# Kernel tuning notes

Measured on AMD Instinct MI355X. Metric: run time of the kernel, lower is better.

Reference implementation:

```python
import jax, jax.numpy as jnp
import numpy as np


def setup_inputs() -> dict:
    key = jax.random.key(0)
    k1, k2, k3 = jax.random.split(key, 3)
    B, T, D, Uh = 64, 256, 1024, 1024
    x = jax.random.normal(k1, (B, T, D), dtype=jnp.float32)
    W = jax.random.normal(k2, (D, 4 * Uh), dtype=jnp.float32) * 0.02
    U = jax.random.normal(k3, (Uh, 4 * Uh), dtype=jnp.float32) * 0.02
    b = jnp.zeros((4 * Uh,), dtype=jnp.float32)
    return {"x": x, "W": W, "U": U, "b": b}


def _lstm(x, W, U, b):
    # Keras LSTM, inference mode (dropout inactive). Gate order: i, f, c, o.
    B = x.shape[0]
    units = U.shape[0]
    # Precompute input projection for all timesteps: [B,T,4U] -> scan over T.
    xz = jnp.einsum('btd,dg->btg', x, W) + b
    xz = jnp.swapaxes(xz, 0, 1)  # [T,B,4U]

    def step(carry, xz_t):
        h, c = carry
        z = xz_t + h @ U  # [B,4U]
        zi, zf, zg, zo = jnp.split(z, 4, axis=-1)
        i = jax.nn.sigmoid(zi)
        f = jax.nn.sigmoid(zf)
        g = jnp.tanh(zg)
        o = jax.nn.sigmoid(zo)
        c_new = f * c + i * g
        h_new = o * jnp.tanh(c_new)
        return (h_new, c_new), h_new

    h0 = jnp.zeros((B, units), dtype=x.dtype)
    c0 = jnp.zeros((B, units), dtype=x.dtype)
    _, hs = jax.lax.scan(step, (h0, c0), xz)  # hs: [T,B,U]
    return jnp.swapaxes(hs, 0, 1)  # [B,T,U] (return_sequences=True)


def reference(x, W, U, b):
    return _lstm(x, W, U, b)
```

## Files before the change

### kernel.cpp

```cpp
#include <hip/hip_runtime.h>
#include <cstdint>
#include <cstddef>

typedef __attribute__((ext_vector_type(8))) short short8;
typedef __attribute__((ext_vector_type(4))) short short4v;
typedef __attribute__((ext_vector_type(4))) float f32x4;

static constexpr int B_ = 64, T_ = 256, D_ = 1024, NH = 1024, NG = 4096;
static constexpr int NBLK = 64;
static constexpr int LDS_BYTES = 131072 + 16384 + 64;

__device__ __forceinline__ short f2bs(float f) {
  union { float f; uint32_t u; } cv; cv.f = f;
  uint32_t u = cv.u;
  uint32_t r = (u + 0x7fffu + ((u >> 16) & 1u)) >> 16;
  return (short)(uint16_t)r;
}
__device__ __forceinline__ float bs2f(short s) {
  union { uint32_t u; float f; } cv; cv.u = ((uint32_t)(uint16_t)s) << 16; return cv.f;
}
__device__ __forceinline__ float fsigm(float x) {
  return __builtin_amdgcn_rcpf(1.f + __expf(-x));
}
__device__ __forceinline__ float ftanh(float x) {
  return 1.f - 2.f * __builtin_amdgcn_rcpf(__expf(2.f * x) + 1.f);
}

__global__ __launch_bounds__(256) void xz_gemm(const float* __restrict__ x,
                                               const float* __restrict__ W,
                                               const float* __restrict__ bias,
                                               short* __restrict__ xzT)
{
  constexpr int BM = 128, BN = 128, BK = 32;
  __shared__ short As[BM][BK];
  __shared__ short Bs[BK][BN];
  __shared__ short Cs[BM][136];
  const int tid  = threadIdx.x;
  const int lane = tid & 63, wave = tid >> 6;
  const int wm = (wave >> 1) * 64, wn = (wave & 1) * 64;
  const int fr = lane & 15, kg = lane >> 4;
  const int bm = blockIdx.x * BM, bn = blockIdx.y * BN;

  f32x4 acc[4][4] = {};

  for (int k0 = 0; k0 < D_; k0 += BK) {
    {
      const int r0 = tid >> 3, kq = (tid & 7) * 4;
      #pragma unroll
      for (int it = 0; it < 4; ++it) {
        const int row = r0 + it * 32;
        const float4 v = *reinterpret_cast<const float4*>(&x[(size_t)(bm + row) * D_ + k0 + kq]);
        short4v s; s.x = f2bs(v.x); s.y = f2bs(v.y); s.z = f2bs(v.z); s.w = f2bs(v.w);
        *reinterpret_cast<short4v*>(&As[row][kq]) = s;
      }
    }
    {
      const int kr0 = tid >> 5, nq = (tid & 31) * 4;
      #pragma unroll
      for (int it = 0; it < 4; ++it) {
        const int krow = kr0 + it * 8;
        const float4 v = *reinterpret_cast<const float4*>(&W[(size_t)(k0 + krow) * NG + bn + nq]);
        short4v s; s.x = f2bs(v.x); s.y = f2bs(v.y); s.z = f2bs(v.z); s.w = f2bs(v.w);
        *reinterpret_cast<short4v*>(&Bs[krow][nq]) = s;
      }
    }
    __syncthreads();

    short8 af[4];
    #pragma unroll
    for (int mi = 0; mi < 4; ++mi)
      af[mi] = *reinterpret_cast<const short8*>(&As[wm + mi * 16 + fr][kg * 8]);
    #pragma unroll
    for (int ni = 0; ni < 4; ++ni) {
      short8 bf;
      #pragma unroll
      for (int j = 0; j < 8; ++j) bf[j] = Bs[kg * 8 + j][wn + ni * 16 + fr];
      #pragma unroll
      for (int mi = 0; mi < 4; ++mi)
        acc[mi][ni] = __builtin_amdgcn_mfma_f32_16x16x32_bf16(af[mi], bf, acc[mi][ni], 0, 0, 0);
    }
    __syncthreads();
  }

  const int fq = lane >> 4;
  #pragma unroll
  for (int ni = 0; ni < 4; ++ni) {
    const int coln = wn + ni * 16 + fr;
    const float bv = bias[bn + coln];
    #pragma unroll
    for (int mi = 0; mi < 4; ++mi) {
      const int rowb = wm + mi * 16 + fq * 4;
      #pragma unroll
      for (int r = 0; r < 4; ++r)
        Cs[rowb + r][coln] = f2bs(acc[mi][ni][r] + bv);
    }
  }
  __syncthreads();

  const int bb  = bm >> 8;
  const int t0  = bm & 255;
  const int g   = bn >> 10;
  const int rb0 = (bn & 1023) >> 4;
  #pragma unroll
  for (int it = 0; it < 4; ++it) {
    const int cid  = it * 256 + tid;
    const int trow = cid >> 3, uu = cid & 7;
    short* dst = xzT + ((size_t)((rb0 + uu) * 256 + (t0 + trow)) * 64 + bb) * 64 + g * 16;
    const short8 v0 = *reinterpret_cast<const short8*>(&Cs[trow][uu * 16]);
    const short8 v1 = *reinterpret_cast<const short8*>(&Cs[trow][uu * 16 + 8]);
    *reinterpret_cast<short8*>(dst)     = v0;
    *reinterpret_cast<short8*>(dst + 8) = v1;
  }
}

#define H_ISSUE(BUF, O0,O1,O2,O3,O4,O5,O6,O7) \
  asm volatile( \
    "global_load_dwordx4 %0, %8, off offset:" #O0 " sc0 sc1\n\t" \
    "global_load_dwordx4 %1, %8, off offset:" #O1 " sc0 sc1\n\t" \
    "global_load_dwordx4 %2, %8, off offset:" #O2 " sc0 sc1\n\t" \
    "global_load_dwordx4 %3, %8, off offset:" #O3 " sc0 sc1\n\t" \
    "global_load_dwordx4 %4, %8, off offset:" #O4 " sc0 sc1\n\t" \
    "global_load_dwordx4 %5, %8, off offset:" #O5 " sc0 sc1\n\t" \
    "global_load_dwordx4 %6, %8, off offset:" #O6 " sc0 sc1" \
    "\n\tglobal_load_dwordx4 %7, %8, off offset:" #O7 " sc0 sc1" \
    : "=&v"(BUF[0]), "=&v"(BUF[1]), "=&v"(BUF[2]), "=&v"(BUF[3]), \
      "=&v"(BUF[4]), "=&v"(BUF[5]), "=&v"(BUF[6]), "=&v"(BUF[7]) \
    : "v"(hp) : "memory")

#define WAITV(N) do { asm volatile("s_waitcnt vmcnt(" #N ")" ::: "memory"); \
                      __builtin_amdgcn_sched_barrier(0); } while (0)

#define LDSWAIT(C) do { \
    while (__hip_atomic_load(&go[C], __ATOMIC_RELAXED, __HIP_MEMORY_SCOPE_WORKGROUP) < t) \
      __builtin_amdgcn_s_sleep(1); \
    __builtin_amdgcn_sched_barrier(0); \
  } while (0)

#define MFMA_CHUNK(BUF, CH) \
  { _Pragma("unroll") \
    for (int i = 0; i < 8; ++i) { \
      const int ksAbs = kh * 16 + (CH) * 8 + i; \
      _Pragma("unroll") \
      for (int nt = 0; nt < 4; ++nt) { \
        const int so = ((ksAbs * 4 + kg) * 64 + nt * 16 + fr) * 8; \
        const short8 bf = *reinterpret_cast<const short8*>(&Us[so]); \
        acc[nt] = __builtin_amdgcn_mfma_f32_16x16x32_bf16(BUF[i], bf, acc[nt], 0, 0, 0); \
      } \
    } }

__global__ __launch_bounds__(576) void lstm_persist(const short* __restrict__ xzT,
                                                    const float* __restrict__ U,
                                                    short* __restrict__ h0buf,
                                                    short* __restrict__ h1buf,
                                                    int* __restrict__ flags,
                                                    float* __restrict__ out)
{
  extern __shared__ char smem[];
  short* Us  = (short*)smem;
  float* zsm = (float*)(smem + 131072);
  int*   go  = (int*)(smem + 131072 + 16384);

  const int tid  = threadIdx.x;
  const int lane = tid & 63, wave = tid >> 6;
  const int bid  = blockIdx.x;
  const int u0   = bid * 16;
  const int fr = lane & 15, kg = lane >> 4;
  const int mt = wave & 3;
  const int kh = wave >> 2;
  const int gb = tid >> 3, gup = tid & 7;

  for (int idx = tid; idx < 1024 * 64; idx += 576) {
    const int k = idx >> 6, c = idx & 63;
    const float v = U[(size_t)k * NG + (c >> 4) * NH + u0 + (c & 15)];
    Us[((k >> 3) * 64 + c) * 8 + (k & 7)] = f2bs(v);
  }
  if (tid < 4) go[tid] = 0;
  float creg0 = 0.f, creg1 = 0.f;
  __syncthreads();

  for (int t = 0; t < T_; ++t) {
    const short* __restrict__ hprev = (t & 1) ? h0buf : h1buf;
    short* __restrict__ hnext       = (t & 1) ? h1buf : h0buf;

    int xzw[4];
    if (tid < 512) {
      const short* xb = xzT + (((size_t)bid * 256 + t) * 64 + gb) * 64;
      #pragma unroll
      for (int g = 0; g < 4; ++g)
        xzw[g] = *reinterpret_cast<const int*>(xb + g * 16 + 2 * gup);
    }

    f32x4 acc[4] = {};
    if (t > 0) {
      if (wave == 8) {
        const int* fp = flags + lane * 16;
        uint32_t pub = 0;
        while (pub != 0xFu) {
          const int v = __hip_atomic_load(fp, __ATOMIC_RELAXED, __HIP_MEMORY_SCOPE_AGENT);
          const unsigned long long rdy = __ballot(v >= t);
          #pragma unroll
          for (int c = 0; c < 4; ++c) {
            if (!((pub >> c) & 1u) && (((rdy >> (c * 16)) & 0xFFFFull) == 0xFFFFull)) {
              if (lane == (unsigned)(c * 16))
                __hip_atomic_store(&go[c], t, __ATOMIC_RELAXED, __HIP_MEMORY_SCOPE_WORKGROUP);
              pub |= 1u << c;
            }
          }
          if (pub != 0xFu) __builtin_amdgcn_s_sleep(1);
        }
      } else {
        const short* hp = hprev + (size_t)(mt * 16 + fr) * NH + kh * 512 + kg * 8;
        short8 ha[8], hb[8];
        LDSWAIT(2 * kh);     H_ISSUE(ha, 0, 64, 128, 192, 256, 320, 384, 448);
        LDSWAIT(2 * kh + 1); H_ISSUE(hb, 512, 576, 640, 704, 768, 832, 896, 960);
        WAITV(8);  MFMA_CHUNK(ha, 0);
        WAITV(0);  MFMA_CHUNK(hb, 1);
        if (kh == 1) {
          #pragma unroll
          for (int nt = 0; nt < 4; ++nt)
            #pragma unroll
            for (int r = 0; r < 4; ++r)
              zsm[(mt * 16 + kg * 4 + r) * 64 + nt * 16 + fr] = acc[nt][r];
        }
      }
      __syncthreads();
      if (wave < 8 && kh == 0) {
        #pragma unroll
        for (int nt = 0; nt < 4; ++nt)
          #pragma unroll
          for (int r = 0; r < 4; ++r) {
            const int zi = (mt * 16 + kg * 4 + r) * 64 + nt * 16 + fr;
            zsm[zi] += acc[nt][r];
          }
      }
      __syncthreads();
    }

    float hh0 = 0.f, hh1 = 0.f;
    if (tid < 512) {
      float z[4][2];
      #pragma unroll
      for (int g = 0; g < 4; ++g) {
        z[g][0] = bs2f((short)(xzw[g] & 0xFFFF));
        z[g][1] = bs2f((short)(((uint32_t)xzw[g]) >> 16));
        if (t > 0) {
          const float2 zz = *reinterpret_cast<const float2*>(&zsm[gb * 64 + g * 16 + 2 * gup]);
          z[g][0] += zz.x; z[g][1] += zz.y;
        }
      }
      {
        const float ig = fsigm(z[0][0]), fg = fsigm(z[1][0]);
        const float gg = ftanh(z[2][0]), og = fsigm(z[3][0]);
        creg0 = fg * creg0 + ig * gg;  hh0 = og * ftanh(creg0);
      }
      {
        const float ig = fsigm(z[0][1]), fg = fsigm(z[1][1]);
        const float gg = ftanh(z[2][1]), og = fsigm(z[3][1]);
        creg1 = fg * creg1 + ig * gg;  hh1 = og * ftanh(creg1);
      }
      if (t < T_ - 1) {
        const uint32_t word = (uint32_t)(uint16_t)f2bs(hh0) | ((uint32_t)(uint16_t)f2bs(hh1) << 16);
        uint32_t* hp32 = (uint32_t*)(hnext + (size_t)gb * NH + u0 + 2 * gup);
        asm volatile("global_store_dword %0, %1, off sc0 sc1" :: "v"(hp32), "v"(word) : "memory");
      }
    }
    if (t < T_ - 1) WAITV(0);
    __syncthreads();

    if (t < T_ - 1 && tid == 0)
      __hip_atomic_store(&flags[bid * 16], t + 1, __ATOMIC_RELAXED, __HIP_MEMORY_SCOPE_AGENT);

    if (tid < 512) {
      float2 o; o.x = hh0; o.y = hh1;
      *reinterpret_cast<float2*>(&out[((size_t)gb * T_ + t) * NH + u0 + 2 * gup]) = o;
    }
  }
}

extern "C" void kernel_launch(void* const* d_in, const int* in_sizes, int n_in,
                              void* d_out, int out_size, void* d_ws, size_t ws_size,
                              hipStream_t stream) {
  const float* x    = (const float*)d_in[0];
  const float* W    = (const float*)d_in[1];
  const float* U    = (const float*)d_in[2];
  const float* bias = (const float*)d_in[3];
  float* out = (float*)d_out;
  char* ws = (char*)d_ws;

  short* xzT   = (short*)ws;
  int*   flags = (int*)(ws + 134217728);
  short* hA    = (short*)(ws + 134225920);
  short* hB    = (short*)(ws + 134356992);

  hipMemsetAsync(flags, 0, 8192, stream);
  xz_gemm<<<dim3(128, 32), 256, 0, stream>>>(x, W, bias, xzT);

  hipFuncSetAttribute((const void*)lstm_persist,
                      hipFuncAttributeMaxDynamicSharedMemorySize, LDS_BYTES);
  lstm_persist<<<dim3(NBLK), dim3(576), LDS_BYTES, stream>>>(xzT, U, hA, hB, flags, out);
}
```

Baseline: 2.109 ms.

## Replace flag-based inter-block sync with timestep-tagged h values polled directly

Removes the per-block flag array and the dedicated polling wave. Each stored h value now carries the timestep in its upper 16 bits, and consumers spin-reload their h fragments until every tag matches. This drops the store-drain wait, the extra block barrier and the flag round-trip on the recurrent critical path, at the cost of doubling the h buffer size and repacking loaded words into bf16 operands. It also pads the z scratch rows to 68 floats to reduce LDS bank conflicts and shrinks the block to 512 threads.

After: 2.292 ms. +8.7%, slower.

```diff
diff --git a/kernel.cpp b/kernel.cpp
--- a/kernel.cpp
+++ b/kernel.cpp
@@ -5,10 +5,12 @@
 typedef __attribute__((ext_vector_type(8))) short short8;
 typedef __attribute__((ext_vector_type(4))) short short4v;
 typedef __attribute__((ext_vector_type(4))) float f32x4;
+typedef __attribute__((ext_vector_type(4))) int int4v;
+typedef __attribute__((ext_vector_type(2))) int int2v;
 
 static constexpr int B_ = 64, T_ = 256, D_ = 1024, NH = 1024, NG = 4096;
 static constexpr int NBLK = 64;
-static constexpr int LDS_BYTES = 131072 + 16384 + 64;
+static constexpr int LDS_BYTES = 131072 + 64 * 68 * 4;
 
 __device__ __forceinline__ short f2bs(float f) {
   union { float f; uint32_t u; } cv; cv.f = f;
@@ -113,52 +115,50 @@
   }
 }
 
-#define H_ISSUE(BUF, O0,O1,O2,O3,O4,O5,O6,O7) \
-  asm volatile( \
-    "global_load_dwordx4 %0, %8, off offset:" #O0 " sc0 sc1\n\t" \
-    "global_load_dwordx4 %1, %8, off offset:" #O1 " sc0 sc1\n\t" \
-    "global_load_dwordx4 %2, %8, off offset:" #O2 " sc0 sc1\n\t" \
-    "global_load_dwordx4 %3, %8, off offset:" #O3 " sc0 sc1\n\t" \
-    "global_load_dwordx4 %4, %8, off offset:" #O4 " sc0 sc1\n\t" \
-    "global_load_dwordx4 %5, %8, off offset:" #O5 " sc0 sc1\n\t" \
-    "global_load_dwordx4 %6, %8, off offset:" #O6 " sc0 sc1" \
-    "\n\tglobal_load_dwordx4 %7, %8, off offset:" #O7 " sc0 sc1" \
-    : "=&v"(BUF[0]), "=&v"(BUF[1]), "=&v"(BUF[2]), "=&v"(BUF[3]), \
-      "=&v"(BUF[4]), "=&v"(BUF[5]), "=&v"(BUF[6]), "=&v"(BUF[7]) \
-    : "v"(hp) : "memory")
-
 #define WAITV(N) do { asm volatile("s_waitcnt vmcnt(" #N ")" ::: "memory"); \
                       __builtin_amdgcn_sched_barrier(0); } while (0)
 
-#define LDSWAIT(C) do { \
-    while (__hip_atomic_load(&go[C], __ATOMIC_RELAXED, __HIP_MEMORY_SCOPE_WORKGROUP) < t) \
-      __builtin_amdgcn_s_sleep(1); \
-    __builtin_amdgcn_sched_barrier(0); \
-  } while (0)
-
-#define MFMA_CHUNK(BUF, CH) \
-  { _Pragma("unroll") \
-    for (int i = 0; i < 8; ++i) { \
-      const int ksAbs = kh * 16 + (CH) * 8 + i; \
-      _Pragma("unroll") \
-      for (int nt = 0; nt < 4; ++nt) { \
-        const int so = ((ksAbs * 4 + kg) * 64 + nt * 16 + fr) * 8; \
-        const short8 bf = *reinterpret_cast<const short8*>(&Us[so]); \
-        acc[nt] = __builtin_amdgcn_mfma_f32_16x16x32_bf16(BUF[i], bf, acc[nt], 0, 0, 0); \
-      } \
-    } }
-
-__global__ __launch_bounds__(576) void lstm_persist(const short* __restrict__ xzT,
-                                                    const float* __restrict__ U,
-                                                    short* __restrict__ h0buf,
-                                                    short* __restrict__ h1buf,
-                                                    int* __restrict__ flags,
-                                                    float* __restrict__ out)
+#define HL2(B0, B1, VO) \
+  asm volatile("global_load_dwordx4 %0, %2, %3 sc0 sc1\n\t" \
+               "global_load_dwordx4 %1, %2, %3 offset:16 sc0 sc1" \
+               : "=&v"(B0), "=&v"(B1) : "v"(VO), "s"(hpv) : "memory")
+
+#define ISSUE_A { _Pragma("unroll") \
+  for (int K = 0; K < 8; ++K) HL2(bufA[2*K], bufA[2*K+1], voff0 + K * 8192); }
+#define ISSUE_B { _Pragma("unroll") \
+  for (int K = 0; K < 8; ++K) HL2(bufB[2*K], bufB[2*K+1], voff0 + 65536 + K * 8192); }
+
+#define CHECKBUF(BUF) { _Pragma("unroll") \
+  for (int i = 0; i < 16; ++i) { \
+    bad |= ((uint32_t)BUF[i][0] ^ tgw); bad |= ((uint32_t)BUF[i][1] ^ tgw); \
+    bad |= ((uint32_t)BUF[i][2] ^ tgw); bad |= ((uint32_t)BUF[i][3] ^ tgw); \
+  } bad &= 0xFFFF0000u; }
+
+#define MFMA_SUB(BUF, KB) { _Pragma("unroll") \
+  for (int K = 0; K < 8; ++K) { \
+    int4v pk; \
+    pk[0] = (BUF[2*K][0]   & 0xFFFF) | (BUF[2*K][1]   << 16); \
+    pk[1] = (BUF[2*K][2]   & 0xFFFF) | (BUF[2*K][3]   << 16); \
+    pk[2] = (BUF[2*K+1][0] & 0xFFFF) | (BUF[2*K+1][1] << 16); \
+    pk[3] = (BUF[2*K+1][2] & 0xFFFF) | (BUF[2*K+1][3] << 16); \
+    const short8 fa = __builtin_bit_cast(short8, pk); \
+    const int ksAbs = kh * 16 + (KB) + K; \
+    _Pragma("unroll") \
+    for (int nt = 0; nt < 4; ++nt) { \
+      const short8 fb = *reinterpret_cast<const short8*>(&Us[((ksAbs*4 + kg)*64 + nt*16 + fr)*8]); \
+      acc[nt] = __builtin_amdgcn_mfma_f32_16x16x32_bf16(fa, fb, acc[nt], 0, 0, 0); \
+    } \
+  } }
+
+__global__ __launch_bounds__(512, 2) void lstm_persist(const short* __restrict__ xzT,
+                                                       const float* __restrict__ U,
+                                                       uint32_t* __restrict__ h0buf,
+                                                       uint32_t* __restrict__ h1buf,
+                                                       float* __restrict__ out)
 {
   extern __shared__ char smem[];
   short* Us  = (short*)smem;
   float* zsm = (float*)(smem + 131072);
-  int*   go  = (int*)(smem + 131072 + 16384);
 
   const int tid  = threadIdx.x;
   const int lane = tid & 63, wave = tid >> 6;
@@ -169,21 +169,22 @@
   const int kh = wave >> 2;
   const int gb = tid >> 3, gup = tid & 7;
 
-  for (int idx = tid; idx < 1024 * 64; idx += 576) {
+  for (int idx = tid; idx < 1024 * 64; idx += 512) {
     const int k = idx >> 6, c = idx & 63;
-    const float v = U[(size_t)k * NG + (c >> 4) * NH + u0 + (c & 15)];
-    Us[((k >> 3) * 64 + c) * 8 + (k & 7)] = f2bs(v);
-  }
-  if (tid < 4) go[tid] = 0;
+    Us[((k >> 3) * 64 + c) * 8 + (k & 7)] =
+        f2bs(U[(size_t)k * NG + (c >> 4) * NH + u0 + (c & 15)]);
+  }
   float creg0 = 0.f, creg1 = 0.f;
+  const int row = mt * 16 + fr;
+  const int voff0 = kh * 131072 + (kg >> 1) * 4096 + row * 64 + (kg & 1) * 32;
   __syncthreads();
 
   for (int t = 0; t < T_; ++t) {
-    const short* __restrict__ hprev = (t & 1) ? h0buf : h1buf;
-    short* __restrict__ hnext       = (t & 1) ? h1buf : h0buf;
+    const uint32_t* __restrict__ hpv = (t & 1) ? h0buf : h1buf;
+    uint32_t* __restrict__ hnx       = (t & 1) ? h1buf : h0buf;
 
     int xzw[4];
-    if (tid < 512) {
+    {
       const short* xb = xzT + (((size_t)bid * 256 + t) * 64 + gb) * 64;
       #pragma unroll
       for (int g = 0; g < 4; ++g)
@@ -192,62 +193,56 @@
 
     f32x4 acc[4] = {};
     if (t > 0) {
-      if (wave == 8) {
-        const int* fp = flags + lane * 16;
-        uint32_t pub = 0;
-        while (pub != 0xFu) {
-          const int v = __hip_atomic_load(fp, __ATOMIC_RELAXED, __HIP_MEMORY_SCOPE_AGENT);
-          const unsigned long long rdy = __ballot(v >= t);
-          #pragma unroll
-          for (int c = 0; c < 4; ++c) {
-            if (!((pub >> c) & 1u) && (((rdy >> (c * 16)) & 0xFFFFull) == 0xFFFFull)) {
-              if (lane == (unsigned)(c * 16))
-                __hip_atomic_store(&go[c], t, __ATOMIC_RELAXED, __HIP_MEMORY_SCOPE_WORKGROUP);
-              pub |= 1u << c;
-            }
-          }
-          if (pub != 0xFu) __builtin_amdgcn_s_sleep(1);
-        }
-      } else {
-        const short* hp = hprev + (size_t)(mt * 16 + fr) * NH + kh * 512 + kg * 8;
-        short8 ha[8], hb[8];
-        LDSWAIT(2 * kh);     H_ISSUE(ha, 0, 64, 128, 192, 256, 320, 384, 448);
-        LDSWAIT(2 * kh + 1); H_ISSUE(hb, 512, 576, 640, 704, 768, 832, 896, 960);
-        WAITV(8);  MFMA_CHUNK(ha, 0);
-        WAITV(0);  MFMA_CHUNK(hb, 1);
-        if (kh == 1) {
-          #pragma unroll
-          for (int nt = 0; nt < 4; ++nt)
-            #pragma unroll
-            for (int r = 0; r < 4; ++r)
-              zsm[(mt * 16 + kg * 4 + r) * 64 + nt * 16 + fr] = acc[nt][r];
-        }
-      }
-      __syncthreads();
-      if (wave < 8 && kh == 0) {
+      const uint32_t tgw = (uint32_t)t << 16;
+      int4v bufA[16], bufB[16];
+      ISSUE_A; ISSUE_B;
+      WAITV(16);
+      for (;;) {
+        uint32_t bad = 0; CHECKBUF(bufA);
+        if (__all(bad == 0)) break;
+        __builtin_amdgcn_s_sleep(2);
+        ISSUE_A; WAITV(0);
+      }
+      MFMA_SUB(bufA, 0);
+      WAITV(0);
+      for (;;) {
+        uint32_t bad = 0; CHECKBUF(bufB);
+        if (__all(bad == 0)) break;
+        __builtin_amdgcn_s_sleep(2);
+        ISSUE_B; WAITV(0);
+      }
+      MFMA_SUB(bufB, 8);
+
+      if (kh == 1) {
         #pragma unroll
         for (int nt = 0; nt < 4; ++nt)
           #pragma unroll
-          for (int r = 0; r < 4; ++r) {
-            const int zi = (mt * 16 + kg * 4 + r) * 64 + nt * 16 + fr;
-            zsm[zi] += acc[nt][r];
-          }
+          for (int r = 0; r < 4; ++r)
+            zsm[(mt * 16 + kg * 4 + r) * 68 + nt * 16 + fr] = acc[nt][r];
       }
       __syncthreads();
-    }
-
-    float hh0 = 0.f, hh1 = 0.f;
-    if (tid < 512) {
+      if (kh == 0) {
+        #pragma unroll
+        for (int nt = 0; nt < 4; ++nt)
+          #pragma unroll
+          for (int r = 0; r < 4; ++r)
+            zsm[(mt * 16 + kg * 4 + r) * 68 + nt * 16 + fr] += acc[nt][r];
+      }
+      __syncthreads();
+    }
+
+    {
       float z[4][2];
       #pragma unroll
       for (int g = 0; g < 4; ++g) {
         z[g][0] = bs2f((short)(xzw[g] & 0xFFFF));
         z[g][1] = bs2f((short)(((uint32_t)xzw[g]) >> 16));
         if (t > 0) {
-          const float2 zz = *reinterpret_cast<const float2*>(&zsm[gb * 64 + g * 16 + 2 * gup]);
+          const float2 zz = *reinterpret_cast<const float2*>(&zsm[gb * 68 + g * 16 + 2 * gup]);
           z[g][0] += zz.x; z[g][1] += zz.y;
         }
       }
+      float hh0, hh1;
       {
         const float ig = fsigm(z[0][0]), fg = fsigm(z[1][0]);
         const float gg = ftanh(z[2][0]), og = fsigm(z[3][0]);
@@ -259,21 +254,18 @@
         creg1 = fg * creg1 + ig * gg;  hh1 = og * ftanh(creg1);
       }
       if (t < T_ - 1) {
-        const uint32_t word = (uint32_t)(uint16_t)f2bs(hh0) | ((uint32_t)(uint16_t)f2bs(hh1) << 16);
-        uint32_t* hp32 = (uint32_t*)(hnext + (size_t)gb * NH + u0 + 2 * gup);
-        asm volatile("global_store_dword %0, %1, off sc0 sc1" :: "v"(hp32), "v"(word) : "memory");
-      }
-    }
-    if (t < T_ - 1) WAITV(0);
-    __syncthreads();
-
-    if (t < T_ - 1 && tid == 0)
-      __hip_atomic_store(&flags[bid * 16], t + 1, __ATOMIC_RELAXED, __HIP_MEMORY_SCOPE_AGENT);
-
-    if (tid < 512) {
+        const uint32_t tgp = (uint32_t)(t + 1) << 16;
+        int2v hw;
+        hw[0] = (int)(tgp | (uint32_t)(uint16_t)f2bs(hh0));
+        hw[1] = (int)(tgp | (uint32_t)(uint16_t)f2bs(hh1));
+        uint32_t* hp32 = hnx + (size_t)bid * 1024 + gb * 16 + 2 * gup;
+        asm volatile("global_store_dwordx2 %0, %1, off sc0 sc1"
+                     :: "v"(hp32), "v"(hw) : "memory");
+      }
       float2 o; o.x = hh0; o.y = hh1;
       *reinterpret_cast<float2*>(&out[((size_t)gb * T_ + t) * NH + u0 + 2 * gup]) = o;
     }
+    __builtin_amdgcn_s_barrier();
   }
 }
 
@@ -287,15 +279,14 @@
   float* out = (float*)d_out;
   char* ws = (char*)d_ws;
 
-  short* xzT   = (short*)ws;
-  int*   flags = (int*)(ws + 134217728);
-  short* hA    = (short*)(ws + 134225920);
-  short* hB    = (short*)(ws + 134356992);
-
-  hipMemsetAsync(flags, 0, 8192, stream);
+  short*    xzT = (short*)ws;
+  uint32_t* hA  = (uint32_t*)(ws + 134217728);
+  uint32_t* hB  = (uint32_t*)(ws + 134217728 + 262144);
+
+  hipMemsetAsync(ws + 134217728, 0, 524288, stream);
   xz_gemm<<<dim3(128, 32), 256, 0, stream>>>(x, W, bias, xzT);
 
   hipFuncSetAttribute((const void*)lstm_persist,
                       hipFuncAttributeMaxDynamicSharedMemorySize, LDS_BYTES);
-  lstm_persist<<<dim3(NBLK), dim3(576), LDS_BYTES, stream>>>(xzT, U, hA, hB, flags, out);
-}
+  lstm_persist<<<dim3(NBLK), dim3(512), LDS_BYTES, stream>>>(xzT, U, hA, hB, out);
+}
```
